# Kernel optimization log

Measured on AMD Instinct MI355X. Metric: run time of the kernel, lower is better.

Reference implementation:

```python
import jax, jax.numpy as jnp
import numpy as np

B = 524288   # batch of agents
N = 64       # neighbors (other agents)
H = 32       # hidden (hardcoded in original via zeros(1,32) and sqrt(32))
V = 256      # vocab_size
SCALE = np.float32(np.sqrt(32.0))  # original divides by sqrt(32) regardless of hidden


def setup_inputs() -> dict:
    key = jax.random.key(0)
    ks = jax.random.split(key, 24)
    lin = lambda k, i, o: (jax.random.normal(k, (i, o), jnp.float32) * (1.0 / np.sqrt(i)))
    inp = {
        'symbol': jax.random.randint(ks[0], (B,), 0, V, jnp.int32),
        'other_hidden': jax.random.normal(ks[1], (N, H), jnp.float32),
        'prev_hidden': jax.random.normal(ks[2], (B, H), jnp.float32),
        'emb': jax.random.normal(ks[3], (V, H), jnp.float32),
        'mem_gate': jnp.zeros((H,), jnp.float32),
        'Wm': lin(ks[4], H, H), 'bm': jnp.zeros((H,), jnp.float32),
        'Wq': lin(ks[5], H, H), 'bq': jnp.zeros((H,), jnp.float32),
        'Wk': lin(ks[6], H, H), 'bk': jnp.zeros((H,), jnp.float32),
        'Wv': lin(ks[7], H, H), 'bv': jnp.zeros((H,), jnp.float32),
        'W1': lin(ks[8], H, H), 'b1': jnp.zeros((H,), jnp.float32),
        'W2': lin(ks[9], H, H), 'b2': jnp.zeros((H,), jnp.float32),
        'W3': lin(ks[10], H, H), 'b3': jnp.zeros((H,), jnp.float32),
        'W4': lin(ks[11], H, H), 'b4': jnp.zeros((H,), jnp.float32),
        'Wa': lin(ks[12], H, 1), 'ba': jnp.zeros((1,), jnp.float32),
        'Ws': lin(ks[13], H, V), 'bs': jnp.zeros((V,), jnp.float32),
        'Wi': lin(ks[14], H, 3), 'bi': jnp.zeros((3,), jnp.float32),
    }
    return inp


def reference(symbol, other_hidden, prev_hidden, emb, mem_gate,
              Wm, bm, Wq, bq, Wk, bk, Wv, bv,
              W1, b1, W2, b2, W3, b3, W4, b4,
              Wa, ba, Ws, bs, Wi, bi):
    # embedding lookup
    h = emb[symbol]                                   # [B, H]
    # gated memory update
    gate = jax.nn.sigmoid(mem_gate)                   # [H]
    mem = jnp.tanh(prev_hidden @ Wm + bm)             # [B, H]
    h = h * (1.0 - gate) + mem * gate
    # social attention over shared neighbor set
    q = h @ Wq + bq                                   # [B, H]
    k = other_hidden @ Wk + bk                        # [N, H]
    v = other_hidden @ Wv + bv                        # [N, H]
    scores = (q @ k.T) / SCALE                        # [B, N]
    weights = jax.nn.softmax(scores, axis=-1)
    h = h + (weights @ v) * 0.3
    for W, b in ((W1, b1), (W2, b2), (W3, b3), (W4, b4)):
        h = h + jnp.tanh(h @ W + b) * 0.3
    # output heads
    action = jnp.tanh(h @ Wa + ba)                    # [B, 1]
    symbol_pred = h @ Ws + bs                         # [B, V]
    intent = h @ Wi + bi                              # [B, 3]
    return (action, symbol_pred, intent, h)
```

## Files before the change

kernel.cpp:

```cpp
#include <hip/hip_runtime.h>
#include <hip/hip_bf16.h>

constexpr int BTOT = 524288;
constexpr int NN   = 64;
constexpr int H    = 32;
constexpr int V    = 256;

typedef __attribute__((ext_vector_type(4))) float f32x4;
typedef __attribute__((ext_vector_type(4))) int   int4v;
typedef __attribute__((ext_vector_type(8))) short short8;

union FragU { int4v i; short8 s; };

__device__ __forceinline__ float fast_rcp(float x){ return __builtin_amdgcn_rcpf(x); }
__device__ __forceinline__ float fast_tanh(float x){
    float e = __expf(2.0f * x);
    return 1.0f - 2.0f * fast_rcp(e + 1.0f);
}
__device__ __forceinline__ int pkbf(float lo, float hi){
    union { __hip_bfloat162 h2; int i; } u;
    u.h2.x = __float2bfloat16(lo);
    u.h2.y = __float2bfloat16(hi);
    return u.i;
}

__device__ __attribute__((aligned(16))) int   g_Wfrag [6*2*64*4];
__device__ __attribute__((aligned(16))) int   g_Kfrag [4*64*4];
__device__ __attribute__((aligned(16))) int   g_Vfrag [2*2*64*4];
__device__ __attribute__((aligned(16))) int   g_Wsfrag[16*64*4];
__device__ __attribute__((aligned(16))) float g_biasd [6*64*8];
__device__ __attribute__((aligned(16))) float g_gated [64*8];
__device__ __attribute__((aligned(16))) float g_wad   [64*8];
__device__ __attribute__((aligned(16))) float g_wid   [64*24];

__global__ void precompute(const float* __restrict__ other_hidden,
                           const float* __restrict__ mem_gate,
                           const float* __restrict__ Wk, const float* __restrict__ bk,
                           const float* __restrict__ Wv, const float* __restrict__ bv,
                           const float* __restrict__ Wm, const float* __restrict__ bm,
                           const float* __restrict__ Wq, const float* __restrict__ bq,
                           const float* __restrict__ W1, const float* __restrict__ b1,
                           const float* __restrict__ W2, const float* __restrict__ b2,
                           const float* __restrict__ W3, const float* __restrict__ b3,
                           const float* __restrict__ W4, const float* __restrict__ b4,
                           const float* __restrict__ Wa, const float* __restrict__ Wi,
                           const float* __restrict__ Ws)
{
    __shared__ float Kst[64][32];
    __shared__ float Vst[64][32];
    __shared__ float gateS[32];
    const int t = threadIdx.x;

    if (t < 32) gateS[t] = fast_rcp(1.0f + __expf(-mem_gate[t]));
    {
        int n = t >> 2, c = (t & 3) * 8;
        float ak[8], av[8];
        #pragma unroll
        for (int i = 0; i < 8; ++i){ ak[i] = bk[c+i]; av[i] = bv[c+i]; }
        #pragma unroll
        for (int j = 0; j < H; ++j){
            float x = other_hidden[n*H + j];
            #pragma unroll
            for (int i = 0; i < 8; ++i){
                ak[i] = fmaf(x, Wk[j*H + c + i], ak[i]);
                av[i] = fmaf(x, Wv[j*H + c + i], av[i]);
            }
        }
        #pragma unroll
        for (int i = 0; i < 8; ++i){ Kst[n][c+i] = ak[i]; Vst[n][c+i] = av[i]; }
    }
    __syncthreads();

    #pragma unroll
    for (int w = 0; w < 6; ++w){
        const float* W = (w==0)?Wm : (w==1)?Wq : (w==2)?W1 : (w==3)?W2 : (w==4)?W3 : W4;
        for (int e = t; e < 128; e += 256){
            int mt = e >> 6, l = e & 63, la = l & 15, g = l >> 4;
            int m = mt*16 + la;
            int base = ((w*2 + mt)*64 + l)*4;
            #pragma unroll
            for (int j = 0; j < 4; ++j){
                int k0 = g*8 + 2*j;
                g_Wfrag[base + j] = pkbf(W[k0*H + m], W[(k0+1)*H + m]);
            }
        }
    }
    #pragma unroll
    for (int w = 0; w < 6; ++w){
        const float* bp_ = (w==0)?bm : (w==1)?bq : (w==2)?b1 : (w==3)?b2 : (w==4)?b3 : b4;
        for (int e = t; e < 512; e += 256){
            int l = e >> 3, idx = e & 7, mt = idx >> 2, r = idx & 3;
            int F = mt*16 + ((l>>4)&3)*4 + r;
            g_biasd[(w*64 + l)*8 + idx] = bp_[F];
        }
    }
    {
        int e = t;
        int mt = e >> 6, l = e & 63, la = l & 15, g = l >> 4;
        int n = mt*16 + la;
        #pragma unroll
        for (int j = 0; j < 4; ++j){
            int k0 = g*8 + 2*j;
            g_Kfrag[e*4 + j] = pkbf(Kst[n][k0], Kst[n][k0+1]);
        }
    }
    {
        int e = t;
        int mt = e >> 7, kt = (e >> 6) & 1, l = e & 63, la = l & 15, g = l >> 4;
        int m = mt*16 + la;
        #pragma unroll
        for (int j = 0; j < 4; ++j){
            int n0 = kt*32 + g*8 + 2*j;
            g_Vfrag[e*4 + j] = pkbf(Vst[n0][m], Vst[n0+1][m]);
        }
    }
    for (int e = t; e < 1024; e += 256){
        int mt = e >> 6, l = e & 63, la = l & 15, g = l >> 4;
        int m = mt*16 + la;
        #pragma unroll
        for (int j = 0; j < 4; ++j){
            int k0 = g*8 + 2*j;
            g_Wsfrag[e*4 + j] = pkbf(Ws[k0*V + m], Ws[(k0+1)*V + m]);
        }
    }
    for (int e = t; e < 512; e += 256){
        int l = e >> 3, idx = e & 7;
        int F = (idx>>2)*16 + ((l>>4)&3)*4 + (idx&3);
        g_gated[e] = gateS[F];
        g_wad[e]   = Wa[F];
    }
    for (int e = t; e < 1536; e += 256){
        int l = e / 24, m2 = e % 24, fidx = m2 / 3, j = m2 % 3;
        int F = (fidx>>2)*16 + ((l>>4)&3)*4 + (fidx&3);
        g_wid[e] = Wi[F*3 + j];
    }
}

__device__ __forceinline__ FragU d2b(f32x4 m0, f32x4 m1, int idxA, int idxB, bool glo){
    int p0a = pkbf(m0[0], m0[1]);
    int p1a = pkbf(m0[2], m0[3]);
    int p0b = pkbf(m1[0], m1[1]);
    int p1b = pkbf(m1[2], m1[3]);
    int tA0  = __builtin_amdgcn_ds_bpermute(idxA, p0a);
    int tA0b = __builtin_amdgcn_ds_bpermute(idxA, p0b);
    int tA1  = __builtin_amdgcn_ds_bpermute(idxA, p1a);
    int tA1b = __builtin_amdgcn_ds_bpermute(idxA, p1b);
    int tB0  = __builtin_amdgcn_ds_bpermute(idxB, p0a);
    int tB0b = __builtin_amdgcn_ds_bpermute(idxB, p0b);
    int tB1  = __builtin_amdgcn_ds_bpermute(idxB, p1a);
    int tB1b = __builtin_amdgcn_ds_bpermute(idxB, p1b);
    FragU r;
    r.i = int4v{ glo ? tA0 : tA0b, glo ? tA1 : tA1b,
                 glo ? tB0 : tB0b, glo ? tB1 : tB1b };
    return r;
}

__device__ __forceinline__ float bred_sum(float v, int bx16, int bx32){
    v += __int_as_float(__builtin_amdgcn_ds_bpermute(bx16, __float_as_int(v)));
    v += __int_as_float(__builtin_amdgcn_ds_bpermute(bx32, __float_as_int(v)));
    return v;
}
__device__ __forceinline__ float bred_max(float v, int bx16, int bx32){
    v = fmaxf(v, __int_as_float(__builtin_amdgcn_ds_bpermute(bx16, __float_as_int(v))));
    v = fmaxf(v, __int_as_float(__builtin_amdgcn_ds_bpermute(bx32, __float_as_int(v))));
    return v;
}
__device__ __forceinline__ f32x4 tanh4(f32x4 v){
    f32x4 r;
    r[0] = fast_tanh(v[0]); r[1] = fast_tanh(v[1]);
    r[2] = fast_tanh(v[2]); r[3] = fast_tanh(v[3]);
    return r;
}

#define MFMA(a, b, c) __builtin_amdgcn_mfma_f32_16x16x32_bf16((a), (b), (c), 0, 0, 0)

__global__ __launch_bounds__(256, 3) void social_main(
    const int*   __restrict__ symbol,
    const float* __restrict__ prev_hidden,
    const float* __restrict__ emb,
    const float* __restrict__ bs,
    const float* __restrict__ ba,
    const float* __restrict__ bi,
    float* __restrict__ out)
{
    const int tid = threadIdx.x;
    const int wv = tid >> 6, l = tid & 63;
    const int la = l & 15, g = l >> 4;
    const bool glo = (g < 2);
    const int idxA = (((g & 1) << 5) + la) << 2;
    const int idxB = idxA + 64;
    const int bx16 = (l ^ 16) << 2;
    const int bx32 = (l ^ 32) << 2;
    const int A0 = blockIdx.x * 128 + wv * 32;

    __shared__ float ldsAll[4][1088];
    __shared__ int4v sSF[1024];
    __shared__ float bsS[256];
    float* lbase = ldsAll[wv];

    {
        const int4v* q4 = reinterpret_cast<const int4v*>(g_Wsfrag);
        for (int i = tid; i < 1024; i += 256) sSF[i] = q4[i];
        bsS[tid] = bs[tid];
    }
    __syncthreads();

    float* out_action = out;
    float* out_sym    = out + (size_t)BTOT;
    float* out_int    = out + (size_t)BTOT * (1 + V);
    float* out_h      = out + (size_t)BTOT * (1 + V + 3);

    const int4v* WF = reinterpret_cast<const int4v*>(g_Wfrag);
    const int4v* KF = reinterpret_cast<const int4v*>(g_Kfrag);
    const int4v* VF = reinterpret_cast<const int4v*>(g_Vfrag);
    const f32x4 zero4 = {0.f, 0.f, 0.f, 0.f};

    FragU phb[2];
    #pragma unroll
    for (int nt = 0; nt < 2; ++nt){
        const f32x4* p = reinterpret_cast<const f32x4*>(
            prev_hidden + (size_t)(A0 + nt*16 + la) * H + g*8);
        f32x4 v0 = p[0], v1 = p[1];
        phb[nt].i = int4v{ pkbf(v0[0],v0[1]), pkbf(v0[2],v0[3]),
                           pkbf(v1[0],v1[1]), pkbf(v1[2],v1[3]) };
    }

    f32x4 h_[2][2];
    {
        f32x4 bias[2];
        bias[0] = *reinterpret_cast<const f32x4*>(g_biasd + l*8);
        bias[1] = *reinterpret_cast<const f32x4*>(g_biasd + l*8 + 4);
        f32x4 m_[2][2];
        #pragma unroll
        for (int mt = 0; mt < 2; ++mt){
            FragU af; af.i = WF[(0*2 + mt)*64 + l];
            #pragma unroll
            for (int nt = 0; nt < 2; ++nt)
                m_[mt][nt] = MFMA(af.s, phb[nt].s, bias[mt]);
        }
        f32x4 gt[2];
        gt[0] = *reinterpret_cast<const f32x4*>(g_gated + l*8);
        gt[1] = *reinterpret_cast<const f32x4*>(g_gated + l*8 + 4);
        int sym0 = symbol[A0 + la], sym1 = symbol[A0 + 16 + la];
        #pragma unroll
        for (int mt = 0; mt < 2; ++mt)
        #pragma unroll
        for (int nt = 0; nt < 2; ++nt){
            const float* eb = emb + (size_t)(nt ? sym1 : sym0)*H + mt*16 + g*4;
            #pragma unroll
            for (int r = 0; r < 4; ++r){
                float gv = gt[mt][r];
                h_[mt][nt][r] = eb[r]*(1.0f - gv) + fast_tanh(m_[mt][nt][r])*gv;
            }
        }
    }

    f32x4 q_[2][2];
    {
        f32x4 bias[2];
        bias[0] = *reinterpret_cast<const f32x4*>(g_biasd + 512 + l*8);
        bias[1] = *reinterpret_cast<const f32x4*>(g_biasd + 512 + l*8 + 4);
        FragU hb[2] = { d2b(h_[0][0], h_[1][0], idxA, idxB, glo),
                        d2b(h_[0][1], h_[1][1], idxA, idxB, glo) };
        #pragma unroll
        for (int mt = 0; mt < 2; ++mt){
            FragU af; af.i = WF[(1*2 + mt)*64 + l];
            #pragma unroll
            for (int nt = 0; nt < 2; ++nt)
                q_[mt][nt] = MFMA(af.s, hb[nt].s, bias[mt]);
        }
    }

    f32x4 s_[4][2];
    {
        FragU qb[2] = { d2b(q_[0][0], q_[1][0], idxA, idxB, glo),
                        d2b(q_[0][1], q_[1][1], idxA, idxB, glo) };
        #pragma unroll
        for (int mt = 0; mt < 4; ++mt){
            FragU af; af.i = KF[mt*64 + l];
            #pragma unroll
            for (int nt = 0; nt < 2; ++nt)
                s_[mt][nt] = MFMA(af.s, qb[nt].s, zero4);
        }
    }

    const float INVS = 0.17677669529663687f;
    float coef[2];
    #pragma unroll
    for (int nt = 0; nt < 2; ++nt){
        float mx = s_[0][nt][0];
        #pragma unroll
        for (int mt = 0; mt < 4; ++mt)
        #pragma unroll
        for (int r = 0; r < 4; ++r) mx = fmaxf(mx, s_[mt][nt][r]);
        mx = bred_max(mx, bx16, bx32);
        float den = 0.f;
        #pragma unroll
        for (int mt = 0; mt < 4; ++mt)
        #pragma unroll
        for (int r = 0; r < 4; ++r){
            float w = __expf((s_[mt][nt][r] - mx) * INVS);
            s_[mt][nt][r] = w;
            den += w;
        }
        den = bred_sum(den, bx16, bx32);
        coef[nt] = 0.3f * fast_rcp(den);
    }

    {
        FragU wb[2][2];
        #pragma unroll
        for (int kt = 0; kt < 2; ++kt)
        #pragma unroll
        for (int nt = 0; nt < 2; ++nt)
            wb[kt][nt] = d2b(s_[2*kt][nt], s_[2*kt+1][nt], idxA, idxB, glo);
        #pragma unroll
        for (int mt = 0; mt < 2; ++mt){
            FragU vf0, vf1;
            vf0.i = VF[(mt*2 + 0)*64 + l];
            vf1.i = VF[(mt*2 + 1)*64 + l];
            #pragma unroll
            for (int nt = 0; nt < 2; ++nt){
                f32x4 acc = MFMA(vf0.s, wb[0][nt].s, zero4);
                acc = MFMA(vf1.s, wb[1][nt].s, acc);
                h_[mt][nt] += acc * coef[nt];
            }
        }
    }

    for (int blk = 0; blk < 4; ++blk){
        f32x4 bias[2];
        bias[0] = *reinterpret_cast<const f32x4*>(g_biasd + (2+blk)*512 + l*8);
        bias[1] = *reinterpret_cast<const f32x4*>(g_biasd + (2+blk)*512 + l*8 + 4);
        FragU hb[2] = { d2b(h_[0][0], h_[1][0], idxA, idxB, glo),
                        d2b(h_[0][1], h_[1][1], idxA, idxB, glo) };
        #pragma unroll
        for (int mt = 0; mt < 2; ++mt){
            FragU af; af.i = WF[((2+blk)*2 + mt)*64 + l];
            #pragma unroll
            for (int nt = 0; nt < 2; ++nt){
                f32x4 tv = MFMA(af.s, hb[nt].s, bias[mt]);
                h_[mt][nt] += 0.3f * tanh4(tv);
            }
        }
    }

    FragU hb[2] = { d2b(h_[0][0], h_[1][0], idxA, idxB, glo),
                    d2b(h_[0][1], h_[1][1], idxA, idxB, glo) };

    {
        union { f32x4 v[2]; float s[8]; } wa;
        wa.v[0] = *reinterpret_cast<const f32x4*>(g_wad + l*8);
        wa.v[1] = *reinterpret_cast<const f32x4*>(g_wad + l*8 + 4);
        float ba0 = ba[0];
        float act[2];
        #pragma unroll
        for (int nt = 0; nt < 2; ++nt){
            float acc = 0.f;
            #pragma unroll
            for (int mt = 0; mt < 2; ++mt)
            #pragma unroll
            for (int r = 0; r < 4; ++r)
                acc = fmaf(h_[mt][nt][r], wa.s[mt*4 + r], acc);
            acc = bred_sum(acc, bx16, bx32);
            act[nt] = fast_tanh(acc + ba0);
        }
        if (l < 16){
            out_action[A0 + la]      = act[0];
            out_action[A0 + 16 + la] = act[1];
        }
    }

    {
        union { f32x4 v[6]; float s[24]; } wi;
        #pragma unroll
        for (int k = 0; k < 6; ++k)
            wi.v[k] = *(reinterpret_cast<const f32x4*>(g_wid + l*24) + k);
        float bi0 = bi[0], bi1 = bi[1], bi2 = bi[2];
        #pragma unroll
        for (int nt = 0; nt < 2; ++nt){
            float i0 = 0.f, i1 = 0.f, i2 = 0.f;
            #pragma unroll
            for (int mt = 0; mt < 2; ++mt)
            #pragma unroll
            for (int r = 0; r < 4; ++r){
                float hv = h_[mt][nt][r];
                int base = (mt*4 + r)*3;
                i0 = fmaf(hv, wi.s[base + 0], i0);
                i1 = fmaf(hv, wi.s[base + 1], i1);
                i2 = fmaf(hv, wi.s[base + 2], i2);
            }
            i0 = bred_sum(i0, bx16, bx32) + bi0;
            i1 = bred_sum(i1, bx16, bx32) + bi1;
            i2 = bred_sum(i2, bx16, bx32) + bi2;
            if (l < 16){
                size_t a = (size_t)(A0 + nt*16 + la);
                out_int[a*3 + 0] = i0;
                out_int[a*3 + 1] = i1;
                out_int[a*3 + 2] = i2;
            }
        }
    }

    {
        float* buf = lbase;
        #pragma unroll
        for (int mt = 0; mt < 2; ++mt)
        #pragma unroll
        for (int nt = 0; nt < 2; ++nt){
            int wb0 = (nt*16 + la)*33 + mt*16 + g*4;
            buf[wb0 + 0] = h_[mt][nt][0];
            buf[wb0 + 1] = h_[mt][nt][1];
            buf[wb0 + 2] = h_[mt][nt][2];
            buf[wb0 + 3] = h_[mt][nt][3];
        }
        int c = l & 7;
        #pragma unroll
        for (int j = 0; j < 4; ++j){
            int ag = j*8 + (l >> 3);
            f32x4 ov;
            ov[0] = buf[ag*33 + c*4 + 0];
            ov[1] = buf[ag*33 + c*4 + 1];
            ov[2] = buf[ag*33 + c*4 + 2];
            ov[3] = buf[ag*33 + c*4 + 3];
            *reinterpret_cast<f32x4*>(out_h + (size_t)(A0 + ag)*H + c*4) = ov;
        }
    }

    {
        int c2 = l & 3, rr = l >> 2;
        #pragma unroll
        for (int mt = 0; mt < 16; ++mt){
            FragU af; af.i = sSF[mt*64 + l];
            f32x4 o0 = MFMA(af.s, hb[0].s, zero4);
            f32x4 o1 = MFMA(af.s, hb[1].s, zero4);
            float* buf = lbase + (mt & 1)*544;
            int w0 = la*17 + g*4;
            int w1 = (16 + la)*17 + g*4;
            buf[w0+0] = o0[0]; buf[w0+1] = o0[1]; buf[w0+2] = o0[2]; buf[w0+3] = o0[3];
            buf[w1+0] = o1[0]; buf[w1+1] = o1[1]; buf[w1+2] = o1[2]; buf[w1+3] = o1[3];
            f32x4 bv = *reinterpret_cast<const f32x4*>(bsS + mt*16 + c2*4);
            #pragma unroll
            for (int j = 0; j < 2; ++j){
                int ag = j*16 + rr;
                f32x4 ov;
                ov[0] = buf[ag*17 + c2*4 + 0] + bv[0];
                ov[1] = buf[ag*17 + c2*4 + 1] + bv[1];
                ov[2] = buf[ag*17 + c2*4 + 2] + bv[2];
                ov[3] = buf[ag*17 + c2*4 + 3] + bv[3];
                *reinterpret_cast<f32x4*>(out_sym + (size_t)(A0 + ag)*V + mt*16 + c2*4) = ov;
            }
        }
    }
}

extern "C" void kernel_launch(void* const* d_in, const int* in_sizes, int n_in,
                              void* d_out, int out_size, void* d_ws, size_t ws_size,
                              hipStream_t stream)
{
    const int*   symbol       = (const int*)  d_in[0];
    const float* other_hidden = (const float*)d_in[1];
    const float* prev_hidden  = (const float*)d_in[2];
    const float* emb          = (const float*)d_in[3];
    const float* mem_gate     = (const float*)d_in[4];
    const float* Wm  = (const float*)d_in[5];  const float* bm = (const float*)d_in[6];
    const float* Wq  = (const float*)d_in[7];  const float* bq = (const float*)d_in[8];
    const float* Wk  = (const float*)d_in[9];  const float* bk = (const float*)d_in[10];
    const float* Wv  = (const float*)d_in[11]; const float* bv = (const float*)d_in[12];
    const float* W1  = (const float*)d_in[13]; const float* b1 = (const float*)d_in[14];
    const float* W2  = (const float*)d_in[15]; const float* b2 = (const float*)d_in[16];
    const float* W3  = (const float*)d_in[17]; const float* b3 = (const float*)d_in[18];
    const float* W4  = (const float*)d_in[19]; const float* b4 = (const float*)d_in[20];
    const float* Wa  = (const float*)d_in[21]; const float* ba = (const float*)d_in[22];
    const float* Wsm = (const float*)d_in[23]; const float* bs = (const float*)d_in[24];
    const float* Wi  = (const float*)d_in[25]; const float* bi = (const float*)d_in[26];

    precompute<<<1, 256, 0, stream>>>(other_hidden, mem_gate, Wk, bk, Wv, bv,
                                      Wm, bm, Wq, bq, W1, b1, W2, b2, W3, b3, W4, b4,
                                      Wa, Wi, Wsm);

    social_main<<<BTOT / 128, 256, 0, stream>>>(symbol, prev_hidden, emb, bs, ba, bi,
                                                (float*)d_out);
}
```

Baseline: 162.7 us.

## Process two 32-agent tiles per wave for more ILP, halving the grid

```diff
diff --git a/kernel.cpp b/kernel.cpp
--- a/kernel.cpp
+++ b/kernel.cpp
@@ -174,7 +174,7 @@
 
 #define MFMA(a, b, c) __builtin_amdgcn_mfma_f32_16x16x32_bf16((a), (b), (c), 0, 0, 0)
 
-__global__ __launch_bounds__(256, 3) void social_main(
+__global__ __launch_bounds__(256, 2) void social_main(
     const int*   __restrict__ symbol,
     const float* __restrict__ prev_hidden,
     const float* __restrict__ emb,
@@ -191,7 +191,7 @@
     const int idxB = idxA + 64;
     const int bx16 = (l ^ 16) << 2;
     const int bx32 = (l ^ 32) << 2;
-    const int A0 = blockIdx.x * 128 + wv * 32;
+    const int A0 = blockIdx.x * 256 + wv * 64;
 
     __shared__ float ldsAll[4][1088];
     __shared__ int4v sSF[1024];
@@ -215,159 +215,203 @@
     const int4v* VF = reinterpret_cast<const int4v*>(g_Vfrag);
     const f32x4 zero4 = {0.f, 0.f, 0.f, 0.f};
 
-    FragU phb[2];
-    #pragma unroll
-    for (int nt = 0; nt < 2; ++nt){
-        const f32x4* p = reinterpret_cast<const f32x4*>(
-            prev_hidden + (size_t)(A0 + nt*16 + la) * H + g*8);
-        f32x4 v0 = p[0], v1 = p[1];
-        phb[nt].i = int4v{ pkbf(v0[0],v0[1]), pkbf(v0[2],v0[3]),
-                           pkbf(v1[0],v1[1]), pkbf(v1[2],v1[3]) };
-    }
-
-    f32x4 h_[2][2];
+    FragU phb[2][2];
+    int sym0[2], sym1[2];
+    #pragma unroll
+    for (int u = 0; u < 2; ++u){
+        #pragma unroll
+        for (int nt = 0; nt < 2; ++nt){
+            const f32x4* p = reinterpret_cast<const f32x4*>(
+                prev_hidden + (size_t)(A0 + u*32 + nt*16 + la) * H + g*8);
+            f32x4 v0 = p[0], v1 = p[1];
+            phb[u][nt].i = int4v{ pkbf(v0[0],v0[1]), pkbf(v0[2],v0[3]),
+                                  pkbf(v1[0],v1[1]), pkbf(v1[2],v1[3]) };
+        }
+        sym0[u] = symbol[A0 + u*32 + la];
+        sym1[u] = symbol[A0 + u*32 + 16 + la];
+    }
+
+    f32x4 h_[2][2][2];
     {
         f32x4 bias[2];
         bias[0] = *reinterpret_cast<const f32x4*>(g_biasd + l*8);
         bias[1] = *reinterpret_cast<const f32x4*>(g_biasd + l*8 + 4);
-        f32x4 m_[2][2];
+        f32x4 m_[2][2][2];
         #pragma unroll
         for (int mt = 0; mt < 2; ++mt){
             FragU af; af.i = WF[(0*2 + mt)*64 + l];
             #pragma unroll
+            for (int u = 0; u < 2; ++u)
+            #pragma unroll
             for (int nt = 0; nt < 2; ++nt)
-                m_[mt][nt] = MFMA(af.s, phb[nt].s, bias[mt]);
+                m_[u][mt][nt] = MFMA(af.s, phb[u][nt].s, bias[mt]);
         }
         f32x4 gt[2];
         gt[0] = *reinterpret_cast<const f32x4*>(g_gated + l*8);
         gt[1] = *reinterpret_cast<const f32x4*>(g_gated + l*8 + 4);
-        int sym0 = symbol[A0 + la], sym1 = symbol[A0 + 16 + la];
+        #pragma unroll
+        for (int u = 0; u < 2; ++u)
         #pragma unroll
         for (int mt = 0; mt < 2; ++mt)
         #pragma unroll
         for (int nt = 0; nt < 2; ++nt){
-            const float* eb = emb + (size_t)(nt ? sym1 : sym0)*H + mt*16 + g*4;
+            const float* eb = emb +
+                (size_t)(nt ? sym1[u] : sym0[u])*H + mt*16 + g*4;
             #pragma unroll
             for (int r = 0; r < 4; ++r){
                 float gv = gt[mt][r];
-                h_[mt][nt][r] = eb[r]*(1.0f - gv) + fast_tanh(m_[mt][nt][r])*gv;
-            }
-        }
-    }
-
-    f32x4 q_[2][2];
+                h_[u][mt][nt][r] = eb[r]*(1.0f - gv)
+                                 + fast_tanh(m_[u][mt][nt][r])*gv;
+            }
+        }
+    }
+
+    f32x4 q_[2][2][2];
     {
         f32x4 bias[2];
         bias[0] = *reinterpret_cast<const f32x4*>(g_biasd + 512 + l*8);
         bias[1] = *reinterpret_cast<const f32x4*>(g_biasd + 512 + l*8 + 4);
-        FragU hb[2] = { d2b(h_[0][0], h_[1][0], idxA, idxB, glo),
-                        d2b(h_[0][1], h_[1][1], idxA, idxB, glo) };
+        FragU hb0[2][2];
+        #pragma unroll
+        for (int u = 0; u < 2; ++u)
+        #pragma unroll
+        for (int nt = 0; nt < 2; ++nt)
+            hb0[u][nt] = d2b(h_[u][0][nt], h_[u][1][nt], idxA, idxB, glo);
         #pragma unroll
         for (int mt = 0; mt < 2; ++mt){
             FragU af; af.i = WF[(1*2 + mt)*64 + l];
             #pragma unroll
+            for (int u = 0; u < 2; ++u)
+            #pragma unroll
             for (int nt = 0; nt < 2; ++nt)
-                q_[mt][nt] = MFMA(af.s, hb[nt].s, bias[mt]);
-        }
-    }
-
-    f32x4 s_[4][2];
-    {
-        FragU qb[2] = { d2b(q_[0][0], q_[1][0], idxA, idxB, glo),
-                        d2b(q_[0][1], q_[1][1], idxA, idxB, glo) };
+                q_[u][mt][nt] = MFMA(af.s, hb0[u][nt].s, bias[mt]);
+        }
+    }
+
+    f32x4 s_[2][4][2];
+    {
+        FragU qb[2][2];
+        #pragma unroll
+        for (int u = 0; u < 2; ++u)
+        #pragma unroll
+        for (int nt = 0; nt < 2; ++nt)
+            qb[u][nt] = d2b(q_[u][0][nt], q_[u][1][nt], idxA, idxB, glo);
         #pragma unroll
         for (int mt = 0; mt < 4; ++mt){
             FragU af; af.i = KF[mt*64 + l];
             #pragma unroll
+            for (int u = 0; u < 2; ++u)
+            #pragma unroll
             for (int nt = 0; nt < 2; ++nt)
-                s_[mt][nt] = MFMA(af.s, qb[nt].s, zero4);
+                s_[u][mt][nt] = MFMA(af.s, qb[u][nt].s, zero4);
         }
     }
 
     const float INVS = 0.17677669529663687f;
-    float coef[2];
+    float coef[2][2];
+    #pragma unroll
+    for (int u = 0; u < 2; ++u)
     #pragma unroll
     for (int nt = 0; nt < 2; ++nt){
-        float mx = s_[0][nt][0];
+        float mx = s_[u][0][nt][0];
         #pragma unroll
         for (int mt = 0; mt < 4; ++mt)
         #pragma unroll
-        for (int r = 0; r < 4; ++r) mx = fmaxf(mx, s_[mt][nt][r]);
+        for (int r = 0; r < 4; ++r) mx = fmaxf(mx, s_[u][mt][nt][r]);
         mx = bred_max(mx, bx16, bx32);
         float den = 0.f;
         #pragma unroll
         for (int mt = 0; mt < 4; ++mt)
         #pragma unroll
         for (int r = 0; r < 4; ++r){
-            float w = __expf((s_[mt][nt][r] - mx) * INVS);
-            s_[mt][nt][r] = w;
+            float w = __expf((s_[u][mt][nt][r] - mx) * INVS);
+            s_[u][mt][nt][r] = w;
             den += w;
         }
         den = bred_sum(den, bx16, bx32);
-        coef[nt] = 0.3f * fast_rcp(den);
-    }
-
-    {
-        FragU wb[2][2];
+        coef[u][nt] = 0.3f * fast_rcp(den);
+    }
+
+    {
+        FragU wb[2][2][2];
+        #pragma unroll
+        for (int u = 0; u < 2; ++u)
         #pragma unroll
         for (int kt = 0; kt < 2; ++kt)
         #pragma unroll
         for (int nt = 0; nt < 2; ++nt)
-            wb[kt][nt] = d2b(s_[2*kt][nt], s_[2*kt+1][nt], idxA, idxB, glo);
+            wb[u][kt][nt] = d2b(s_[u][2*kt][nt], s_[u][2*kt+1][nt],
+                                idxA, idxB, glo);
         #pragma unroll
         for (int mt = 0; mt < 2; ++mt){
             FragU vf0, vf1;
             vf0.i = VF[(mt*2 + 0)*64 + l];
             vf1.i = VF[(mt*2 + 1)*64 + l];
             #pragma unroll
+            for (int u = 0; u < 2; ++u)
+            #pragma unroll
             for (int nt = 0; nt < 2; ++nt){
-                f32x4 acc = MFMA(vf0.s, wb[0][nt].s, zero4);
-                acc = MFMA(vf1.s, wb[1][nt].s, acc);
-                h_[mt][nt] += acc * coef[nt];
-            }
-        }
-    }
-
+                f32x4 acc = MFMA(vf0.s, wb[u][0][nt].s, zero4);
+                acc = MFMA(vf1.s, wb[u][1][nt].s, acc);
+                h_[u][mt][nt] += acc * coef[u][nt];
+            }
+        }
+    }
+
+    #pragma unroll 1
     for (int blk = 0; blk < 4; ++blk){
         f32x4 bias[2];
         bias[0] = *reinterpret_cast<const f32x4*>(g_biasd + (2+blk)*512 + l*8);
         bias[1] = *reinterpret_cast<const f32x4*>(g_biasd + (2+blk)*512 + l*8 + 4);
-        FragU hb[2] = { d2b(h_[0][0], h_[1][0], idxA, idxB, glo),
-                        d2b(h_[0][1], h_[1][1], idxA, idxB, glo) };
+        FragU hb1[2][2];
+        #pragma unroll
+        for (int u = 0; u < 2; ++u)
+        #pragma unroll
+        for (int nt = 0; nt < 2; ++nt)
+            hb1[u][nt] = d2b(h_[u][0][nt], h_[u][1][nt], idxA, idxB, glo);
         #pragma unroll
         for (int mt = 0; mt < 2; ++mt){
             FragU af; af.i = WF[((2+blk)*2 + mt)*64 + l];
             #pragma unroll
+            for (int u = 0; u < 2; ++u)
+            #pragma unroll
             for (int nt = 0; nt < 2; ++nt){
-                f32x4 tv = MFMA(af.s, hb[nt].s, bias[mt]);
-                h_[mt][nt] += 0.3f * tanh4(tv);
-            }
-        }
-    }
-
-    FragU hb[2] = { d2b(h_[0][0], h_[1][0], idxA, idxB, glo),
-                    d2b(h_[0][1], h_[1][1], idxA, idxB, glo) };
+                f32x4 tv = MFMA(af.s, hb1[u][nt].s, bias[mt]);
+                h_[u][mt][nt] += 0.3f * tanh4(tv);
+            }
+        }
+    }
+
+    FragU hb[2][2];
+    #pragma unroll
+    for (int u = 0; u < 2; ++u)
+    #pragma unroll
+    for (int nt = 0; nt < 2; ++nt)
+        hb[u][nt] = d2b(h_[u][0][nt], h_[u][1][nt], idxA, idxB, glo);
 
     {
         union { f32x4 v[2]; float s[8]; } wa;
         wa.v[0] = *reinterpret_cast<const f32x4*>(g_wad + l*8);
         wa.v[1] = *reinterpret_cast<const f32x4*>(g_wad + l*8 + 4);
         float ba0 = ba[0];
-        float act[2];
-        #pragma unroll
-        for (int nt = 0; nt < 2; ++nt){
-            float acc = 0.f;
-            #pragma unroll
-            for (int mt = 0; mt < 2; ++mt)
-            #pragma unroll
-            for (int r = 0; r < 4; ++r)
-                acc = fmaf(h_[mt][nt][r], wa.s[mt*4 + r], acc);
-            acc = bred_sum(acc, bx16, bx32);
-            act[nt] = fast_tanh(acc + ba0);
-        }
-        if (l < 16){
-            out_action[A0 + la]      = act[0];
-            out_action[A0 + 16 + la] = act[1];
+        #pragma unroll
+        for (int u = 0; u < 2; ++u){
+            float act[2];
+            #pragma unroll
+            for (int nt = 0; nt < 2; ++nt){
+                float acc = 0.f;
+                #pragma unroll
+                for (int mt = 0; mt < 2; ++mt)
+                #pragma unroll
+                for (int r = 0; r < 4; ++r)
+                    acc = fmaf(h_[u][mt][nt][r], wa.s[mt*4 + r], acc);
+                acc = bred_sum(acc, bx16, bx32);
+                act[nt] = fast_tanh(acc + ba0);
+            }
+            if (l < 16){
+                out_action[A0 + u*32 + la]      = act[0];
+                out_action[A0 + u*32 + 16 + la] = act[1];
+            }
         }
     }
 
@@ -378,13 +422,15 @@
             wi.v[k] = *(reinterpret_cast<const f32x4*>(g_wid + l*24) + k);
         float bi0 = bi[0], bi1 = bi[1], bi2 = bi[2];
         #pragma unroll
+        for (int u = 0; u < 2; ++u)
+        #pragma unroll
         for (int nt = 0; nt < 2; ++nt){
             float i0 = 0.f, i1 = 0.f, i2 = 0.f;
             #pragma unroll
             for (int mt = 0; mt < 2; ++mt)
             #pragma unroll
             for (int r = 0; r < 4; ++r){
-                float hv = h_[mt][nt][r];
+                float hv = h_[u][mt][nt][r];
                 int base = (mt*4 + r)*3;
                 i0 = fmaf(hv, wi.s[base + 0], i0);
                 i1 = fmaf(hv, wi.s[base + 1], i1);
@@ -394,7 +440,7 @@
             i1 = bred_sum(i1, bx16, bx32) + bi1;
             i2 = bred_sum(i2, bx16, bx32) + bi2;
             if (l < 16){
-                size_t a = (size_t)(A0 + nt*16 + la);
+                size_t a = (size_t)(A0 + u*32 + nt*16 + la);
                 out_int[a*3 + 0] = i0;
                 out_int[a*3 + 1] = i1;
                 out_int[a*3 + 2] = i2;
@@ -402,17 +448,18 @@
         }
     }
 
-    {
+    #pragma unroll
+    for (int u = 0; u < 2; ++u){
         float* buf = lbase;
         #pragma unroll
         for (int mt = 0; mt < 2; ++mt)
         #pragma unroll
         for (int nt = 0; nt < 2; ++nt){
             int wb0 = (nt*16 + la)*33 + mt*16 + g*4;
-            buf[wb0 + 0] = h_[mt][nt][0];
-            buf[wb0 + 1] = h_[mt][nt][1];
-            buf[wb0 + 2] = h_[mt][nt][2];
-            buf[wb0 + 3] = h_[mt][nt][3];
+            buf[wb0 + 0] = h_[u][mt][nt][0];
+            buf[wb0 + 1] = h_[u][mt][nt][1];
+            buf[wb0 + 2] = h_[u][mt][nt][2];
+            buf[wb0 + 3] = h_[u][mt][nt][3];
         }
         int c = l & 7;
         #pragma unroll
@@ -423,32 +470,39 @@
             ov[1] = buf[ag*33 + c*4 + 1];
             ov[2] = buf[ag*33 + c*4 + 2];
             ov[3] = buf[ag*33 + c*4 + 3];
-            *reinterpret_cast<f32x4*>(out_h + (size_t)(A0 + ag)*H + c*4) = ov;
+            *reinterpret_cast<f32x4*>(
+                out_h + (size_t)(A0 + u*32 + ag)*H + c*4) = ov;
         }
     }
 
     {
         int c2 = l & 3, rr = l >> 2;
         #pragma unroll
-        for (int mt = 0; mt < 16; ++mt){
-            FragU af; af.i = sSF[mt*64 + l];
-            f32x4 o0 = MFMA(af.s, hb[0].s, zero4);
-            f32x4 o1 = MFMA(af.s, hb[1].s, zero4);
-            float* buf = lbase + (mt & 1)*544;
-            int w0 = la*17 + g*4;
-            int w1 = (16 + la)*17 + g*4;
-            buf[w0+0] = o0[0]; buf[w0+1] = o0[1]; buf[w0+2] = o0[2]; buf[w0+3] = o0[3];
-            buf[w1+0] = o1[0]; buf[w1+1] = o1[1]; buf[w1+2] = o1[2]; buf[w1+3] = o1[3];
-            f32x4 bv = *reinterpret_cast<const f32x4*>(bsS + mt*16 + c2*4);
-            #pragma unroll
-            for (int j = 0; j < 2; ++j){
-                int ag = j*16 + rr;
-                f32x4 ov;
-                ov[0] = buf[ag*17 + c2*4 + 0] + bv[0];
-                ov[1] = buf[ag*17 + c2*4 + 1] + bv[1];
-                ov[2] = buf[ag*17 + c2*4 + 2] + bv[2];
-                ov[3] = buf[ag*17 + c2*4 + 3] + bv[3];
-                *reinterpret_cast<f32x4*>(out_sym + (size_t)(A0 + ag)*V + mt*16 + c2*4) = ov;
+        for (int u = 0; u < 2; ++u){
+            #pragma unroll
+            for (int mt = 0; mt < 16; ++mt){
+                FragU af; af.i = sSF[mt*64 + l];
+                f32x4 o0 = MFMA(af.s, hb[u][0].s, zero4);
+                f32x4 o1 = MFMA(af.s, hb[u][1].s, zero4);
+                float* buf = lbase + (mt & 1)*544;
+                int w0 = la*17 + g*4;
+                int w1 = (16 + la)*17 + g*4;
+                buf[w0+0] = o0[0]; buf[w0+1] = o0[1];
+                buf[w0+2] = o0[2]; buf[w0+3] = o0[3];
+                buf[w1+0] = o1[0]; buf[w1+1] = o1[1];
+                buf[w1+2] = o1[2]; buf[w1+3] = o1[3];
+                f32x4 bv = *reinterpret_cast<const f32x4*>(bsS + mt*16 + c2*4);
+                #pragma unroll
+                for (int j = 0; j < 2; ++j){
+                    int ag = j*16 + rr;
+                    f32x4 ov;
+                    ov[0] = buf[ag*17 + c2*4 + 0] + bv[0];
+                    ov[1] = buf[ag*17 + c2*4 + 1] + bv[1];
+                    ov[2] = buf[ag*17 + c2*4 + 2] + bv[2];
+                    ov[3] = buf[ag*17 + c2*4 + 3] + bv[3];
+                    *reinterpret_cast<f32x4*>(
+                        out_sym + (size_t)(A0 + u*32 + ag)*V + mt*16 + c2*4) = ov;
+                }
             }
         }
     }
@@ -479,6 +533,6 @@
                                       Wm, bm, Wq, bq, W1, b1, W2, b2, W3, b3, W4, b4,
                                       Wa, Wi, Wsm);
 
-    social_main<<<BTOT / 128, 256, 0, stream>>>(symbol, prev_hidden, emb, bs, ba, bi,
+    social_main<<<BTOT / 256, 256, 0, stream>>>(symbol, prev_hidden, emb, bs, ba, bi,
                                                 (float*)d_out);
 }
```

Measured after the change: 171.1 us. 5.2% more time.

## Process two agent tiles per block with prefetch of the next tile's inputs

Applied to the files above, without the earlier changes.

```diff
diff --git a/kernel.cpp b/kernel.cpp
--- a/kernel.cpp
+++ b/kernel.cpp
@@ -191,12 +191,11 @@
     const int idxB = idxA + 64;
     const int bx16 = (l ^ 16) << 2;
     const int bx32 = (l ^ 32) << 2;
-    const int A0 = blockIdx.x * 128 + wv * 32;
+    const int base = blockIdx.x * 256 + wv * 32;
 
     __shared__ float ldsAll[4][1088];
     __shared__ int4v sSF[1024];
     __shared__ float bsS[256];
-    float* lbase = ldsAll[wv];
 
     {
         const int4v* q4 = reinterpret_cast<const int4v*>(g_Wsfrag);
@@ -204,6 +203,7 @@
         bsS[tid] = bs[tid];
     }
     __syncthreads();
+    float* lbase = ldsAll[wv];
 
     float* out_action = out;
     float* out_sym    = out + (size_t)BTOT;
@@ -215,240 +215,284 @@
     const int4v* VF = reinterpret_cast<const int4v*>(g_Vfrag);
     const f32x4 zero4 = {0.f, 0.f, 0.f, 0.f};
 
-    FragU phb[2];
+    FragU phbA[2][2];
+    f32x4 emA[2][2][2];
+    int symN0, symN1;
+
+    {
+        #pragma unroll
+        for (int nt = 0; nt < 2; ++nt){
+            const f32x4* p = reinterpret_cast<const f32x4*>(
+                prev_hidden + (size_t)(base + nt*16 + la) * H + g*8);
+            f32x4 v0 = p[0], v1 = p[1];
+            phbA[0][nt].i = int4v{ pkbf(v0[0],v0[1]), pkbf(v0[2],v0[3]),
+                                   pkbf(v1[0],v1[1]), pkbf(v1[2],v1[3]) };
+        }
+        int s0 = symbol[base + la], s1 = symbol[base + 16 + la];
+        symN0 = symbol[base + 128 + la];
+        symN1 = symbol[base + 128 + 16 + la];
+        #pragma unroll
+        for (int mt = 0; mt < 2; ++mt)
+        #pragma unroll
+        for (int nt = 0; nt < 2; ++nt)
+            emA[0][mt][nt] = *reinterpret_cast<const f32x4*>(
+                emb + (size_t)(nt ? s1 : s0)*H + mt*16 + g*4);
+    }
+
     #pragma unroll
-    for (int nt = 0; nt < 2; ++nt){
-        const f32x4* p = reinterpret_cast<const f32x4*>(
-            prev_hidden + (size_t)(A0 + nt*16 + la) * H + g*8);
-        f32x4 v0 = p[0], v1 = p[1];
-        phb[nt].i = int4v{ pkbf(v0[0],v0[1]), pkbf(v0[2],v0[3]),
-                           pkbf(v1[0],v1[1]), pkbf(v1[2],v1[3]) };
-    }
-
-    f32x4 h_[2][2];
-    {
-        f32x4 bias[2];
-        bias[0] = *reinterpret_cast<const f32x4*>(g_biasd + l*8);
-        bias[1] = *reinterpret_cast<const f32x4*>(g_biasd + l*8 + 4);
-        f32x4 m_[2][2];
-        #pragma unroll
-        for (int mt = 0; mt < 2; ++mt){
-            FragU af; af.i = WF[(0*2 + mt)*64 + l];
+    for (int t = 0; t < 2; ++t){
+        const int A0 = base + t*128;
+
+        f32x4 pvr[2][2];
+        if (t == 0){
+            #pragma unroll
+            for (int nt = 0; nt < 2; ++nt){
+                const f32x4* p = reinterpret_cast<const f32x4*>(
+                    prev_hidden + (size_t)(base + 128 + nt*16 + la) * H + g*8);
+                pvr[nt][0] = p[0]; pvr[nt][1] = p[1];
+            }
+        }
+
+        f32x4 h_[2][2];
+        {
+            f32x4 bias[2];
+            bias[0] = *reinterpret_cast<const f32x4*>(g_biasd + l*8);
+            bias[1] = *reinterpret_cast<const f32x4*>(g_biasd + l*8 + 4);
+            f32x4 m_[2][2];
+            #pragma unroll
+            for (int mt = 0; mt < 2; ++mt){
+                FragU af; af.i = WF[(0*2 + mt)*64 + l];
+                #pragma unroll
+                for (int nt = 0; nt < 2; ++nt)
+                    m_[mt][nt] = MFMA(af.s, phbA[t][nt].s, bias[mt]);
+            }
+            f32x4 gt[2];
+            gt[0] = *reinterpret_cast<const f32x4*>(g_gated + l*8);
+            gt[1] = *reinterpret_cast<const f32x4*>(g_gated + l*8 + 4);
+            #pragma unroll
+            for (int mt = 0; mt < 2; ++mt)
+            #pragma unroll
+            for (int nt = 0; nt < 2; ++nt){
+                #pragma unroll
+                for (int r = 0; r < 4; ++r){
+                    float gv = gt[mt][r];
+                    h_[mt][nt][r] = emA[t][mt][nt][r]*(1.0f - gv)
+                                  + fast_tanh(m_[mt][nt][r])*gv;
+                }
+            }
+        }
+
+        f32x4 q_[2][2];
+        {
+            f32x4 bias[2];
+            bias[0] = *reinterpret_cast<const f32x4*>(g_biasd + 512 + l*8);
+            bias[1] = *reinterpret_cast<const f32x4*>(g_biasd + 512 + l*8 + 4);
+            FragU hb0[2] = { d2b(h_[0][0], h_[1][0], idxA, idxB, glo),
+                             d2b(h_[0][1], h_[1][1], idxA, idxB, glo) };
+            #pragma unroll
+            for (int mt = 0; mt < 2; ++mt){
+                FragU af; af.i = WF[(1*2 + mt)*64 + l];
+                #pragma unroll
+                for (int nt = 0; nt < 2; ++nt)
+                    q_[mt][nt] = MFMA(af.s, hb0[nt].s, bias[mt]);
+            }
+        }
+
+        f32x4 s_[4][2];
+        {
+            FragU qb[2] = { d2b(q_[0][0], q_[1][0], idxA, idxB, glo),
+                            d2b(q_[0][1], q_[1][1], idxA, idxB, glo) };
+            #pragma unroll
+            for (int mt = 0; mt < 4; ++mt){
+                FragU af; af.i = KF[mt*64 + l];
+                #pragma unroll
+                for (int nt = 0; nt < 2; ++nt)
+                    s_[mt][nt] = MFMA(af.s, qb[nt].s, zero4);
+            }
+        }
+
+        if (t == 0){
+            #pragma unroll
+            for (int mt = 0; mt < 2; ++mt)
             #pragma unroll
             for (int nt = 0; nt < 2; ++nt)
-                m_[mt][nt] = MFMA(af.s, phb[nt].s, bias[mt]);
-        }
-        f32x4 gt[2];
-        gt[0] = *reinterpret_cast<const f32x4*>(g_gated + l*8);
-        gt[1] = *reinterpret_cast<const f32x4*>(g_gated + l*8 + 4);
-        int sym0 = symbol[A0 + la], sym1 = symbol[A0 + 16 + la];
-        #pragma unroll
-        for (int mt = 0; mt < 2; ++mt)
+                emA[1][mt][nt] = *reinterpret_cast<const f32x4*>(
+                    emb + (size_t)(nt ? symN1 : symN0)*H + mt*16 + g*4);
+            #pragma unroll
+            for (int nt = 0; nt < 2; ++nt)
+                phbA[1][nt].i = int4v{ pkbf(pvr[nt][0][0], pvr[nt][0][1]),
+                                       pkbf(pvr[nt][0][2], pvr[nt][0][3]),
+                                       pkbf(pvr[nt][1][0], pvr[nt][1][1]),
+                                       pkbf(pvr[nt][1][2], pvr[nt][1][3]) };
+        }
+
+        const float INVS = 0.17677669529663687f;
+        float coef[2];
         #pragma unroll
         for (int nt = 0; nt < 2; ++nt){
-            const float* eb = emb + (size_t)(nt ? sym1 : sym0)*H + mt*16 + g*4;
+            float mx = s_[0][nt][0];
+            #pragma unroll
+            for (int mt = 0; mt < 4; ++mt)
+            #pragma unroll
+            for (int r = 0; r < 4; ++r) mx = fmaxf(mx, s_[mt][nt][r]);
+            mx = bred_max(mx, bx16, bx32);
+            float den = 0.f;
+            #pragma unroll
+            for (int mt = 0; mt < 4; ++mt)
             #pragma unroll
             for (int r = 0; r < 4; ++r){
-                float gv = gt[mt][r];
-                h_[mt][nt][r] = eb[r]*(1.0f - gv) + fast_tanh(m_[mt][nt][r])*gv;
-            }
-        }
-    }
-
-    f32x4 q_[2][2];
-    {
-        f32x4 bias[2];
-        bias[0] = *reinterpret_cast<const f32x4*>(g_biasd + 512 + l*8);
-        bias[1] = *reinterpret_cast<const f32x4*>(g_biasd + 512 + l*8 + 4);
+                float w = __expf((s_[mt][nt][r] - mx) * INVS);
+                s_[mt][nt][r] = w;
+                den += w;
+            }
+            den = bred_sum(den, bx16, bx32);
+            coef[nt] = 0.3f * fast_rcp(den);
+        }
+
+        {
+            FragU wb[2][2];
+            #pragma unroll
+            for (int kt = 0; kt < 2; ++kt)
+            #pragma unroll
+            for (int nt = 0; nt < 2; ++nt)
+                wb[kt][nt] = d2b(s_[2*kt][nt], s_[2*kt+1][nt], idxA, idxB, glo);
+            #pragma unroll
+            for (int mt = 0; mt < 2; ++mt){
+                FragU vf0, vf1;
+                vf0.i = VF[(mt*2 + 0)*64 + l];
+                vf1.i = VF[(mt*2 + 1)*64 + l];
+                #pragma unroll
+                for (int nt = 0; nt < 2; ++nt){
+                    f32x4 acc = MFMA(vf0.s, wb[0][nt].s, zero4);
+                    acc = MFMA(vf1.s, wb[1][nt].s, acc);
+                    h_[mt][nt] += acc * coef[nt];
+                }
+            }
+        }
+
+        #pragma unroll 1
+        for (int blk = 0; blk < 4; ++blk){
+            f32x4 bias[2];
+            bias[0] = *reinterpret_cast<const f32x4*>(g_biasd + (2+blk)*512 + l*8);
+            bias[1] = *reinterpret_cast<const f32x4*>(g_biasd + (2+blk)*512 + l*8 + 4);
+            FragU hb1[2] = { d2b(h_[0][0], h_[1][0], idxA, idxB, glo),
+                             d2b(h_[0][1], h_[1][1], idxA, idxB, glo) };
+            #pragma unroll
+            for (int mt = 0; mt < 2; ++mt){
+                FragU af; af.i = WF[((2+blk)*2 + mt)*64 + l];
+                #pragma unroll
+                for (int nt = 0; nt < 2; ++nt){
+                    f32x4 tv = MFMA(af.s, hb1[nt].s, bias[mt]);
+                    h_[mt][nt] += 0.3f * tanh4(tv);
+                }
+            }
+        }
+
         FragU hb[2] = { d2b(h_[0][0], h_[1][0], idxA, idxB, glo),
                         d2b(h_[0][1], h_[1][1], idxA, idxB, glo) };
-        #pragma unroll
-        for (int mt = 0; mt < 2; ++mt){
-            FragU af; af.i = WF[(1*2 + mt)*64 + l];
-            #pragma unroll
-            for (int nt = 0; nt < 2; ++nt)
-                q_[mt][nt] = MFMA(af.s, hb[nt].s, bias[mt]);
-        }
-    }
-
-    f32x4 s_[4][2];
-    {
-        FragU qb[2] = { d2b(q_[0][0], q_[1][0], idxA, idxB, glo),
-                        d2b(q_[0][1], q_[1][1], idxA, idxB, glo) };
-        #pragma unroll
-        for (int mt = 0; mt < 4; ++mt){
-            FragU af; af.i = KF[mt*64 + l];
-            #pragma unroll
-            for (int nt = 0; nt < 2; ++nt)
-                s_[mt][nt] = MFMA(af.s, qb[nt].s, zero4);
-        }
-    }
-
-    const float INVS = 0.17677669529663687f;
-    float coef[2];
-    #pragma unroll
-    for (int nt = 0; nt < 2; ++nt){
-        float mx = s_[0][nt][0];
-        #pragma unroll
-        for (int mt = 0; mt < 4; ++mt)
-        #pragma unroll
-        for (int r = 0; r < 4; ++r) mx = fmaxf(mx, s_[mt][nt][r]);
-        mx = bred_max(mx, bx16, bx32);
-        float den = 0.f;
-        #pragma unroll
-        for (int mt = 0; mt < 4; ++mt)
-        #pragma unroll
-        for (int r = 0; r < 4; ++r){
-            float w = __expf((s_[mt][nt][r] - mx) * INVS);
-            s_[mt][nt][r] = w;
-            den += w;
-        }
-        den = bred_sum(den, bx16, bx32);
-        coef[nt] = 0.3f * fast_rcp(den);
-    }
-
-    {
-        FragU wb[2][2];
-        #pragma unroll
-        for (int kt = 0; kt < 2; ++kt)
-        #pragma unroll
-        for (int nt = 0; nt < 2; ++nt)
-            wb[kt][nt] = d2b(s_[2*kt][nt], s_[2*kt+1][nt], idxA, idxB, glo);
-        #pragma unroll
-        for (int mt = 0; mt < 2; ++mt){
-            FragU vf0, vf1;
-            vf0.i = VF[(mt*2 + 0)*64 + l];
-            vf1.i = VF[(mt*2 + 1)*64 + l];
+
+        {
+            union { f32x4 v[2]; float s[8]; } wa;
+            wa.v[0] = *reinterpret_cast<const f32x4*>(g_wad + l*8);
+            wa.v[1] = *reinterpret_cast<const f32x4*>(g_wad + l*8 + 4);
+            float ba0 = ba[0];
+            float act[2];
             #pragma unroll
             for (int nt = 0; nt < 2; ++nt){
-                f32x4 acc = MFMA(vf0.s, wb[0][nt].s, zero4);
-                acc = MFMA(vf1.s, wb[1][nt].s, acc);
-                h_[mt][nt] += acc * coef[nt];
-            }
-        }
-    }
-
-    for (int blk = 0; blk < 4; ++blk){
-        f32x4 bias[2];
-        bias[0] = *reinterpret_cast<const f32x4*>(g_biasd + (2+blk)*512 + l*8);
-        bias[1] = *reinterpret_cast<const f32x4*>(g_biasd + (2+blk)*512 + l*8 + 4);
-        FragU hb[2] = { d2b(h_[0][0], h_[1][0], idxA, idxB, glo),
-                        d2b(h_[0][1], h_[1][1], idxA, idxB, glo) };
-        #pragma unroll
-        for (int mt = 0; mt < 2; ++mt){
-            FragU af; af.i = WF[((2+blk)*2 + mt)*64 + l];
+                float acc = 0.f;
+                #pragma unroll
+                for (int mt = 0; mt < 2; ++mt)
+                #pragma unroll
+                for (int r = 0; r < 4; ++r)
+                    acc = fmaf(h_[mt][nt][r], wa.s[mt*4 + r], acc);
+                acc = bred_sum(acc, bx16, bx32);
+                act[nt] = fast_tanh(acc + ba0);
+            }
+            if (l < 16){
+                out_action[A0 + la]      = act[0];
+                out_action[A0 + 16 + la] = act[1];
+            }
+        }
+
+        {
+            union { f32x4 v[6]; float s[24]; } wi;
+            #pragma unroll
+            for (int k = 0; k < 6; ++k)
+                wi.v[k] = *(reinterpret_cast<const f32x4*>(g_wid + l*24) + k);
+            float bi0 = bi[0], bi1 = bi[1], bi2 = bi[2];
             #pragma unroll
             for (int nt = 0; nt < 2; ++nt){
-                f32x4 tv = MFMA(af.s, hb[nt].s, bias[mt]);
-                h_[mt][nt] += 0.3f * tanh4(tv);
-            }
-        }
-    }
-
-    FragU hb[2] = { d2b(h_[0][0], h_[1][0], idxA, idxB, glo),
-                    d2b(h_[0][1], h_[1][1], idxA, idxB, glo) };
-
-    {
-        union { f32x4 v[2]; float s[8]; } wa;
-        wa.v[0] = *reinterpret_cast<const f32x4*>(g_wad + l*8);
-        wa.v[1] = *reinterpret_cast<const f32x4*>(g_wad + l*8 + 4);
-        float ba0 = ba[0];
-        float act[2];
-        #pragma unroll
-        for (int nt = 0; nt < 2; ++nt){
-            float acc = 0.f;
+                float i0 = 0.f, i1 = 0.f, i2 = 0.f;
+                #pragma unroll
+                for (int mt = 0; mt < 2; ++mt)
+                #pragma unroll
+                for (int r = 0; r < 4; ++r){
+                    float hv = h_[mt][nt][r];
+                    int bidx = (mt*4 + r)*3;
+                    i0 = fmaf(hv, wi.s[bidx + 0], i0);
+                    i1 = fmaf(hv, wi.s[bidx + 1], i1);
+                    i2 = fmaf(hv, wi.s[bidx + 2], i2);
+                }
+                i0 = bred_sum(i0, bx16, bx32) + bi0;
+                i1 = bred_sum(i1, bx16, bx32) + bi1;
+                i2 = bred_sum(i2, bx16, bx32) + bi2;
+                if (l < 16){
+                    size_t a = (size_t)(A0 + nt*16 + la);
+                    out_int[a*3 + 0] = i0;
+                    out_int[a*3 + 1] = i1;
+                    out_int[a*3 + 2] = i2;
+                }
+            }
+        }
+
+        {
+            float* buf = lbase;
             #pragma unroll
             for (int mt = 0; mt < 2; ++mt)
             #pragma unroll
-            for (int r = 0; r < 4; ++r)
-                acc = fmaf(h_[mt][nt][r], wa.s[mt*4 + r], acc);
-            acc = bred_sum(acc, bx16, bx32);
-            act[nt] = fast_tanh(acc + ba0);
-        }
-        if (l < 16){
-            out_action[A0 + la]      = act[0];
-            out_action[A0 + 16 + la] = act[1];
-        }
-    }
-
-    {
-        union { f32x4 v[6]; float s[24]; } wi;
-        #pragma unroll
-        for (int k = 0; k < 6; ++k)
-            wi.v[k] = *(reinterpret_cast<const f32x4*>(g_wid + l*24) + k);
-        float bi0 = bi[0], bi1 = bi[1], bi2 = bi[2];
-        #pragma unroll
-        for (int nt = 0; nt < 2; ++nt){
-            float i0 = 0.f, i1 = 0.f, i2 = 0.f;
-            #pragma unroll
-            for (int mt = 0; mt < 2; ++mt)
-            #pragma unroll
-            for (int r = 0; r < 4; ++r){
-                float hv = h_[mt][nt][r];
-                int base = (mt*4 + r)*3;
-                i0 = fmaf(hv, wi.s[base + 0], i0);
-                i1 = fmaf(hv, wi.s[base + 1], i1);
-                i2 = fmaf(hv, wi.s[base + 2], i2);
-            }
-            i0 = bred_sum(i0, bx16, bx32) + bi0;
-            i1 = bred_sum(i1, bx16, bx32) + bi1;
-            i2 = bred_sum(i2, bx16, bx32) + bi2;
-            if (l < 16){
-                size_t a = (size_t)(A0 + nt*16 + la);
-                out_int[a*3 + 0] = i0;
-                out_int[a*3 + 1] = i1;
-                out_int[a*3 + 2] = i2;
-            }
-        }
-    }
-
-    {
-        float* buf = lbase;
-        #pragma unroll
-        for (int mt = 0; mt < 2; ++mt)
-        #pragma unroll
-        for (int nt = 0; nt < 2; ++nt){
-            int wb0 = (nt*16 + la)*33 + mt*16 + g*4;
-            buf[wb0 + 0] = h_[mt][nt][0];
-            buf[wb0 + 1] = h_[mt][nt][1];
-            buf[wb0 + 2] = h_[mt][nt][2];
-            buf[wb0 + 3] = h_[mt][nt][3];
-        }
-        int c = l & 7;
-        #pragma unroll
-        for (int j = 0; j < 4; ++j){
-            int ag = j*8 + (l >> 3);
-            f32x4 ov;
-            ov[0] = buf[ag*33 + c*4 + 0];
-            ov[1] = buf[ag*33 + c*4 + 1];
-            ov[2] = buf[ag*33 + c*4 + 2];
-            ov[3] = buf[ag*33 + c*4 + 3];
-            *reinterpret_cast<f32x4*>(out_h + (size_t)(A0 + ag)*H + c*4) = ov;
-        }
-    }
-
-    {
-        int c2 = l & 3, rr = l >> 2;
-        #pragma unroll
-        for (int mt = 0; mt < 16; ++mt){
-            FragU af; af.i = sSF[mt*64 + l];
-            f32x4 o0 = MFMA(af.s, hb[0].s, zero4);
-            f32x4 o1 = MFMA(af.s, hb[1].s, zero4);
-            float* buf = lbase + (mt & 1)*544;
-            int w0 = la*17 + g*4;
-            int w1 = (16 + la)*17 + g*4;
-            buf[w0+0] = o0[0]; buf[w0+1] = o0[1]; buf[w0+2] = o0[2]; buf[w0+3] = o0[3];
-            buf[w1+0] = o1[0]; buf[w1+1] = o1[1]; buf[w1+2] = o1[2]; buf[w1+3] = o1[3];
-            f32x4 bv = *reinterpret_cast<const f32x4*>(bsS + mt*16 + c2*4);
-            #pragma unroll
-            for (int j = 0; j < 2; ++j){
-                int ag = j*16 + rr;
+            for (int nt = 0; nt < 2; ++nt){
+                int wb0 = (nt*16 + la)*33 + mt*16 + g*4;
+                buf[wb0 + 0] = h_[mt][nt][0];
+                buf[wb0 + 1] = h_[mt][nt][1];
+                buf[wb0 + 2] = h_[mt][nt][2];
+                buf[wb0 + 3] = h_[mt][nt][3];
+            }
+            int c = l & 7;
+            #pragma unroll
+            for (int j = 0; j < 4; ++j){
+                int ag = j*8 + (l >> 3);
                 f32x4 ov;
-                ov[0] = buf[ag*17 + c2*4 + 0] + bv[0];
-                ov[1] = buf[ag*17 + c2*4 + 1] + bv[1];
-                ov[2] = buf[ag*17 + c2*4 + 2] + bv[2];
-                ov[3] = buf[ag*17 + c2*4 + 3] + bv[3];
-                *reinterpret_cast<f32x4*>(out_sym + (size_t)(A0 + ag)*V + mt*16 + c2*4) = ov;
+                ov[0] = buf[ag*33 + c*4 + 0];
+                ov[1] = buf[ag*33 + c*4 + 1];
+                ov[2] = buf[ag*33 + c*4 + 2];
+                ov[3] = buf[ag*33 + c*4 + 3];
+                *reinterpret_cast<f32x4*>(out_h + (size_t)(A0 + ag)*H + c*4) = ov;
+            }
+        }
+
+        {
+            int c2 = l & 3, rr = l >> 2;
+            #pragma unroll
+            for (int mt = 0; mt < 16; ++mt){
+                FragU af; af.i = sSF[mt*64 + l];
+                f32x4 o0 = MFMA(af.s, hb[0].s, zero4);
+                f32x4 o1 = MFMA(af.s, hb[1].s, zero4);
+                float* buf = lbase + (mt & 1)*544;
+                int w0 = la*17 + g*4;
+                int w1 = (16 + la)*17 + g*4;
+                buf[w0+0] = o0[0]; buf[w0+1] = o0[1]; buf[w0+2] = o0[2]; buf[w0+3] = o0[3];
+                buf[w1+0] = o1[0]; buf[w1+1] = o1[1]; buf[w1+2] = o1[2]; buf[w1+3] = o1[3];
+                f32x4 bv = *reinterpret_cast<const f32x4*>(bsS + mt*16 + c2*4);
+                #pragma unroll
+                for (int j = 0; j < 2; ++j){
+                    int ag = j*16 + rr;
+                    f32x4 ov;
+                    ov[0] = buf[ag*17 + c2*4 + 0] + bv[0];
+                    ov[1] = buf[ag*17 + c2*4 + 1] + bv[1];
+                    ov[2] = buf[ag*17 + c2*4 + 2] + bv[2];
+                    ov[3] = buf[ag*17 + c2*4 + 3] + bv[3];
+                    *reinterpret_cast<f32x4*>(out_sym + (size_t)(A0 + ag)*V + mt*16 + c2*4) = ov;
+                }
             }
         }
     }
@@ -479,6 +523,6 @@
                                       Wm, bm, Wq, bq, W1, b1, W2, b2, W3, b3, W4, b4,
                                       Wa, Wi, Wsm);
 
-    social_main<<<BTOT / 128, 256, 0, stream>>>(symbol, prev_hidden, emb, bs, ba, bi,
+    social_main<<<BTOT / 256, 256, 0, stream>>>(symbol, prev_hidden, emb, bs, ba, bi,
                                                 (float*)d_out);
 }
```

After: 185.8 us. 1.14x slower.
